# Performance work log

Hardware: AMD Instinct MI355X
Metric: run time of the kernel (lower is better)

The kernel has to match this reference:

```python
import math
import jax, jax.numpy as jnp
import numpy as np

OLEN = 512
RATIO = 0.5
DROP_P = 0.2


def _gat(x, src, dst, W, a_s, a_d, b):
    """PyG GATConv (heads=1, concat=True, add_self_loops=True, neg_slope=0.2)."""
    n = x.shape[0]
    loops = jnp.arange(n, dtype=src.dtype)
    s = jnp.concatenate([src, loops])  # [E+N] source nodes
    d = jnp.concatenate([dst, loops])  # [E+N] destination nodes
    h = x @ W                           # [N, H]
    alpha_s = h @ a_s                   # [N]
    alpha_d = h @ a_d                   # [N]
    e = jax.nn.leaky_relu(alpha_s[s] + alpha_d[d], 0.2)  # [E+N]
    # segment softmax over destination neighborhoods
    m = jax.ops.segment_max(e, d, num_segments=n)
    ee = jnp.exp(e - m[d])
    denom = jax.ops.segment_sum(ee, d, num_segments=n)
    alpha = ee / denom[d]
    out = jax.ops.segment_sum(alpha[:, None] * h[s], d, num_segments=n)
    return out + b


def _forward(x, src, dst, W1, a_src1, a_dst1, b1, W2, a_src2, a_dst2, b2,
             W3, a_src3, a_dst3, b3, W_rel, W_root, b_pool):
    N, E = x.shape[0], src.shape[0]
    key = jax.random.key(42)
    h = x
    for i, (W, a_s, a_d, b) in enumerate([(W1, a_src1, a_dst1, b1),
                                          (W2, a_src2, a_dst2, b2),
                                          (W3, a_src3, a_dst3, b3)]):
        h = jax.nn.relu(_gat(h, src, dst, W, a_s, a_d, b))
        keep = jax.random.bernoulli(jax.random.fold_in(key, i), 1.0 - DROP_P, h.shape)
        h = jnp.where(keep, h / (1.0 - DROP_P), 0.0)  # F.dropout(training=True)

    # SAGPooling(GraphConv score, ratio=0.5, tanh) repeated until n <= 512.
    # Node counts are static per iteration (k = ceil(0.5*n)); edge arrays keep
    # fixed size E with a validity mask (edges dropped when an endpoint is pooled away).
    cur_src, cur_dst = src, dst
    emask = jnp.ones((E,), dtype=h.dtype)
    n = N
    while True:
        agg = jax.ops.segment_sum(h[cur_src] * emask[:, None], cur_dst, num_segments=n)
        score = (agg @ W_rel + h @ W_root + b_pool)[:, 0]  # GraphConv(d->1), aggr='add'
        score = jnp.tanh(score)
        k = math.ceil(RATIO * n)
        top_vals, perm = jax.lax.top_k(score, k)
        h = h[perm] * top_vals[:, None]
        inv = jnp.full((n,), -1, dtype=cur_src.dtype).at[perm].set(
            jnp.arange(k, dtype=cur_src.dtype))
        ns, nd = inv[cur_src], inv[cur_dst]
        valid = (ns >= 0) & (nd >= 0)
        emask = emask * valid.astype(emask.dtype)
        cur_src = jnp.where(valid, ns, 0)
        cur_dst = jnp.where(valid, nd, 0)
        n = k
        if n <= OLEN:
            break

    out = jnp.zeros((OLEN, h.shape[1]), h.dtype).at[:n].set(h)
    return out


def setup_inputs() -> dict:
    key = jax.random.key(0)
    ks = jax.random.split(key, 20)
    N, E, IDIM, HDIM = 50000, 800000, 128, 200
    inp = {
        "x": jax.random.normal(ks[0], (N, IDIM), jnp.float32),
        "src": jax.random.randint(ks[1], (E,), 0, N, jnp.int32),
        "dst": jax.random.randint(ks[2], (E,), 0, N, jnp.int32),
    }
    def w(k, shape, fan_in):
        return jax.random.normal(k, shape, jnp.float32) / np.sqrt(fan_in).astype(np.float32)
    inp["W1"] = w(ks[3], (IDIM, HDIM), IDIM)
    inp["a_src1"] = w(ks[4], (HDIM,), HDIM)
    inp["a_dst1"] = w(ks[5], (HDIM,), HDIM)
    inp["b1"] = jnp.zeros((HDIM,), jnp.float32)
    inp["W2"] = w(ks[6], (HDIM, HDIM), HDIM)
    inp["a_src2"] = w(ks[7], (HDIM,), HDIM)
    inp["a_dst2"] = w(ks[8], (HDIM,), HDIM)
    inp["b2"] = jnp.zeros((HDIM,), jnp.float32)
    inp["W3"] = w(ks[9], (HDIM, HDIM), HDIM)
    inp["a_src3"] = w(ks[10], (HDIM,), HDIM)
    inp["a_dst3"] = w(ks[11], (HDIM,), HDIM)
    inp["b3"] = jnp.zeros((HDIM,), jnp.float32)
    inp["W_rel"] = w(ks[12], (HDIM, 1), HDIM)
    inp["W_root"] = w(ks[13], (HDIM, 1), HDIM)
    inp["b_pool"] = jnp.zeros((1,), jnp.float32)
    return inp


def reference(x, src, dst, W1, a_src1, a_dst1, b1, W2, a_src2, a_dst2, b2,
              W3, a_src3, a_dst3, b3, W_rel, W_root, b_pool):
    return _forward(x, src, dst, W1, a_src1, a_dst1, b1, W2, a_src2, a_dst2, b2,
                    W3, a_src3, a_dst3, b3, W_rel, W_root, b_pool)
```

## Files before the change

kernel.cpp:

```cpp
#include <hip/hip_runtime.h>
#include <cstdint>
#include <cstddef>


__host__ __device__ inline void tf_round(uint32_t &x0, uint32_t &x1, int r) {
  x0 += x1;
  x1 = (x1 << r) | (x1 >> (32 - r));
  x1 ^= x0;
}

__host__ __device__ inline void threefry2x32(uint32_t k0, uint32_t k1,
                                             uint32_t &x0, uint32_t &x1) {
  uint32_t ks2 = k0 ^ k1 ^ 0x1BD11BDAu;
  x0 += k0; x1 += k1;
  tf_round(x0, x1, 13); tf_round(x0, x1, 15); tf_round(x0, x1, 26); tf_round(x0, x1, 6);
  x0 += k1; x1 += ks2 + 1u;
  tf_round(x0, x1, 17); tf_round(x0, x1, 29); tf_round(x0, x1, 16); tf_round(x0, x1, 24);
  x0 += ks2; x1 += k0 + 2u;
  tf_round(x0, x1, 13); tf_round(x0, x1, 15); tf_round(x0, x1, 26); tf_round(x0, x1, 6);
  x0 += k0; x1 += k1 + 3u;
  tf_round(x0, x1, 17); tf_round(x0, x1, 29); tf_round(x0, x1, 16); tf_round(x0, x1, 24);
  x0 += k1; x1 += ks2 + 4u;
  tf_round(x0, x1, 13); tf_round(x0, x1, 15); tf_round(x0, x1, 26); tf_round(x0, x1, 6);
  x0 += ks2; x1 += k0 + 5u;
}

__global__ __launch_bounds__(256) void gemm200_k(
    const float* __restrict__ A, const float* __restrict__ B,
    float* __restrict__ C, int M, int K) {
  __shared__ float As[128 * 9];
  __shared__ __align__(16) float Bs[8][208];
  int tid = threadIdx.x;
  int m0 = blockIdx.x * 128;
  int r = tid >> 2;
  int colBase = (tid & 3) * 52;
  int nq = (colBase == 156) ? 11 : 13;
  float acc0[52], acc1[52];
#pragma unroll
  for (int q = 0; q < 52; q++) { acc0[q] = 0.f; acc1[q] = 0.f; }

  int arow = tid >> 1;
  int ac = (tid & 1) * 4;
  int gmA = m0 + arow;
  const float* Aptr = A + (size_t)gmA * K + ac;
  int bk0 = tid / 50, bc0 = (tid - bk0 * 50) * 4;
  int t2 = tid + 256;
  int bk1 = t2 / 50, bc1 = (t2 - bk1 * 50) * 4;
  bool hasB1 = (t2 < 400);

  float4 va = make_float4(0.f, 0.f, 0.f, 0.f);
  if (gmA < M) va = *(const float4*)(Aptr);
  float4 vb0 = *(const float4*)(B + (size_t)bk0 * 200 + bc0);
  float4 vb1 = make_float4(0.f, 0.f, 0.f, 0.f);
  if (hasB1) vb1 = *(const float4*)(B + (size_t)bk1 * 200 + bc1);

  for (int k0 = 0; k0 < K; k0 += 8) {
    As[arow * 9 + ac + 0] = va.x;
    As[arow * 9 + ac + 1] = va.y;
    As[arow * 9 + ac + 2] = va.z;
    As[arow * 9 + ac + 3] = va.w;
    *(float4*)(&Bs[bk0][bc0]) = vb0;
    if (hasB1) *(float4*)(&Bs[bk1][bc1]) = vb1;
    __syncthreads();
    int kn = k0 + 8;
    if (kn < K) {
      if (gmA < M) va = *(const float4*)(Aptr + kn);
      vb0 = *(const float4*)(B + (size_t)(kn + bk0) * 200 + bc0);
      if (hasB1) vb1 = *(const float4*)(B + (size_t)(kn + bk1) * 200 + bc1);
    }
#pragma unroll
    for (int kk = 0; kk < 8; kk++) {
      float a0 = As[r * 9 + kk];
      float a1 = As[(r + 64) * 9 + kk];
#pragma unroll
      for (int q = 0; q < 13; q++) {
        float4 b = *(const float4*)(&Bs[kk][colBase + 4 * q]);
        acc0[4 * q + 0] += a0 * b.x; acc0[4 * q + 1] += a0 * b.y;
        acc0[4 * q + 2] += a0 * b.z; acc0[4 * q + 3] += a0 * b.w;
        acc1[4 * q + 0] += a1 * b.x; acc1[4 * q + 1] += a1 * b.y;
        acc1[4 * q + 2] += a1 * b.z; acc1[4 * q + 3] += a1 * b.w;
      }
    }
    __syncthreads();
  }
  int gm0 = m0 + r, gm1 = m0 + r + 64;
#pragma unroll
  for (int q = 0; q < 13; q++) {
    if (q < nq) {
      int col = colBase + 4 * q;
      float4 v0 = make_float4(acc0[4 * q + 0], acc0[4 * q + 1],
                              acc0[4 * q + 2], acc0[4 * q + 3]);
      float4 v1 = make_float4(acc1[4 * q + 0], acc1[4 * q + 1],
                              acc1[4 * q + 2], acc1[4 * q + 3]);
      if (gm0 < M) *(float4*)(C + (size_t)gm0 * 200 + col) = v0;
      if (gm1 < M) *(float4*)(C + (size_t)gm1 * 200 + col) = v1;
    }
  }
}

__global__ __launch_bounds__(256) void dual_dot_k(
    const float* __restrict__ H, const float* __restrict__ v1,
    const float* __restrict__ v2, float* __restrict__ o1,
    float* __restrict__ o2, int n) {
  int wave = blockIdx.x * 4 + (threadIdx.x >> 6);
  int lane = threadIdx.x & 63;
  if (wave >= n) return;
  const float* row = H + (size_t)wave * 200;
  float s1 = 0.f, s2 = 0.f;
  for (int d = lane; d < 200; d += 64) {
    float h = row[d];
    s1 += h * v1[d];
    s2 += h * v2[d];
  }
  for (int off = 32; off; off >>= 1) {
    s1 += __shfl_down(s1, off);
    s2 += __shfl_down(s2, off);
  }
  if (lane == 0) { o1[wave] = s1; o2[wave] = s2; }
}

__global__ __launch_bounds__(256) void indeg_k(const int* __restrict__ dst,
                                               int* __restrict__ cnt, int E) {
  int e = blockIdx.x * 256 + threadIdx.x;
  if (e < E) atomicAdd(&cnt[dst[e]], 1);
}

__global__ __launch_bounds__(256) void scan_k(const int* __restrict__ cnt,
                                              int* __restrict__ rowptr, int N) {
  __shared__ int psum[256];
  int t = threadIdx.x;
  int CH = (N + 255) / 256;
  int beg = t * CH, end = min(beg + CH, N);
  if (beg > N) { beg = N; }
  int s = 0;
  for (int i = beg; i < end; i++) s += cnt[i];
  psum[t] = s;
  __syncthreads();
  if (t == 0) {
    int run = 0;
    for (int i = 0; i < 256; i++) { int v = psum[i]; psum[i] = run; run += v; }
  }
  __syncthreads();
  int run = psum[t];
  for (int i = beg; i < end; i++) { rowptr[i] = run; run += cnt[i]; }
  if (end == N && beg <= N) rowptr[N] = run;
}

__global__ __launch_bounds__(256) void cpyint_k(const int* __restrict__ a,
                                                int* __restrict__ b, int n) {
  int i = blockIdx.x * 256 + threadIdx.x;
  if (i < n) b[i] = a[i];
}

__global__ __launch_bounds__(256) void place_k(const int* __restrict__ dst,
                                               int* __restrict__ curs,
                                               int* __restrict__ csr, int E) {
  int e = blockIdx.x * 256 + threadIdx.x;
  if (e >= E) return;
  int pos = atomicAdd(&curs[dst[e]], 1);
  csr[pos] = e;
}

__global__ __launch_bounds__(256) void sortrow_k(const int* __restrict__ rowptr,
                                                 int* __restrict__ csr, int N) {
  int d = blockIdx.x * 256 + threadIdx.x;
  if (d >= N) return;
  int b = rowptr[d], e2 = rowptr[d + 1];
  for (int i = b + 1; i < e2; i++) {
    int v = csr[i];
    int j = i - 1;
    while (j >= b && csr[j] > v) { csr[j + 1] = csr[j]; j--; }
    csr[j + 1] = v;
  }
}

__device__ inline float dec_ord(unsigned enc) {
  unsigned b = (enc & 0x80000000u) ? (enc ^ 0x80000000u) : ~enc;
  return __uint_as_float(b);
}

__global__ __launch_bounds__(256) void edge_max_k(
    const int* __restrict__ src, const int* __restrict__ dst,
    const float* __restrict__ as_, const float* __restrict__ ad_,
    unsigned* __restrict__ menc, int E, int N) {
  int j = blockIdx.x * 256 + threadIdx.x;
  if (j >= E + N) return;
  int s, d;
  if (j < E) { s = src[j]; d = dst[j]; } else { s = j - E; d = s; }
  float v = as_[s] + ad_[d];
  float ev = (v >= 0.f) ? v : 0.2f * v;
  unsigned b = __float_as_uint(ev);
  unsigned enc = (b & 0x80000000u) ? ~b : (b | 0x80000000u);
  atomicMax(&menc[d], enc);
}

__global__ __launch_bounds__(256) void ee_k(
    const int* __restrict__ src, const int* __restrict__ dst,
    const float* __restrict__ as_, const float* __restrict__ ad_,
    const unsigned* __restrict__ menc, float* __restrict__ ee, int E, int N) {
  int j = blockIdx.x * 256 + threadIdx.x;
  if (j >= E + N) return;
  int s, d;
  if (j < E) { s = src[j]; d = dst[j]; } else { s = j - E; d = s; }
  float v = as_[s] + ad_[d];
  float ev = (v >= 0.f) ? v : 0.2f * v;
  ee[j] = expf(ev - dec_ord(menc[d]));
}

__global__ __launch_bounds__(256) void den_k(const int* __restrict__ rowptr,
                                             const int* __restrict__ csr,
                                             const float* __restrict__ ee,
                                             float* __restrict__ den, int E, int N) {
  int d = blockIdx.x * 256 + threadIdx.x;
  if (d >= N) return;
  float s = 0.f;
  int b = rowptr[d], e2 = rowptr[d + 1];
  for (int i = b; i < e2; i++) s = __fadd_rn(s, ee[csr[i]]);
  s = __fadd_rn(s, ee[E + d]);
  den[d] = s;
}

__global__ __launch_bounds__(256) void alpha_k(const int* __restrict__ dst,
                                               const float* __restrict__ den,
                                               float* __restrict__ ee, int E, int N) {
  int j = blockIdx.x * 256 + threadIdx.x;
  if (j >= E + N) return;
  int d = (j < E) ? dst[j] : (j - E);
  ee[j] = ee[j] / den[d];
}

__global__ __launch_bounds__(256) void gat_out_k(
    const int* __restrict__ rowptr, const int* __restrict__ csr,
    const int* __restrict__ src, const float* __restrict__ alpha,
    const float* __restrict__ HW, float* __restrict__ OUT, int E, int N) {
  int node = blockIdx.x * 4 + (threadIdx.x >> 6);
  int lane = threadIdx.x & 63;
  if (node >= N || lane >= 50) return;
  int b = rowptr[node];
  int deg = rowptr[node + 1] - b;
  int cnt = deg + 1;

  auto fetchS = [&](int t, int &s, float &w) {
    if (t < deg) {
      int e = csr[b + t];
      s = src[e];
      w = alpha[e];
    } else if (t == deg) {
      s = node;
      w = alpha[E + node];
    } else {
      s = node;
      w = 0.f;
    }
  };

  int s0, s1, s2;
  float w0, w1, w2;
  fetchS(0, s0, w0);
  fetchS(1, s1, w1);
  fetchS(2, s2, w2);
  float4 h0 = *(const float4*)(HW + (size_t)s0 * 200 + 4 * lane);
  float4 h1 = *(const float4*)(HW + (size_t)s1 * 200 + 4 * lane);
  float4 acc = make_float4(0.f, 0.f, 0.f, 0.f);
  for (int t = 0; t < cnt; t++) {
    int s3;
    float w3;
    fetchS(t + 3, s3, w3);
    float4 h2 = *(const float4*)(HW + (size_t)s2 * 200 + 4 * lane);
    acc.x = __fadd_rn(acc.x, __fmul_rn(w0, h0.x));
    acc.y = __fadd_rn(acc.y, __fmul_rn(w0, h0.y));
    acc.z = __fadd_rn(acc.z, __fmul_rn(w0, h0.z));
    acc.w = __fadd_rn(acc.w, __fmul_rn(w0, h0.w));
    h0 = h1; h1 = h2;
    w0 = w1; w1 = w2; w2 = w3;
    s2 = s3;
  }
  *(float4*)(OUT + (size_t)node * 200 + 4 * lane) = acc;
}

__global__ __launch_bounds__(256) void epi_k(float* __restrict__ H,
                                             const float* __restrict__ bias,
                                             uint32_t k0, uint32_t k1, int total) {
  int t = blockIdx.x * 256 + threadIdx.x;
  if (t >= total) return;
  uint32_t x0 = 0u, x1 = (uint32_t)t;
  threefry2x32(k0, k1, x0, x1);
  uint32_t bits = x0 ^ x1;
  float u = __uint_as_float((bits >> 9) | 0x3f800000u) - 1.0f;
  int col = t % 200;
  float v = H[t] + bias[col];
  v = fmaxf(v, 0.f);
  H[t] = (u < 0.8f) ? (v / 0.8f) : 0.f;
}

__global__ __launch_bounds__(256) void einit_k(
    const int* __restrict__ src, const int* __restrict__ dst,
    int* __restrict__ cs, int* __restrict__ cd, int* __restrict__ orig,
    int E, int N) {
  int e = blockIdx.x * 256 + threadIdx.x;
  if (e < E) { cs[e] = src[e]; cd[e] = dst[e]; }
  if (e < N) orig[e] = e;
}

__global__ __launch_bounds__(256) void pool_agg_k(
    const int* __restrict__ rowptr, const int* __restrict__ csr,
    const int* __restrict__ csrc, const int* __restrict__ orig,
    const float* __restrict__ H, float* __restrict__ AGG, int n) {
  int node = blockIdx.x * 4 + (threadIdx.x >> 6);
  int lane = threadIdx.x & 63;
  if (node >= n || lane >= 50) return;
  int o = orig[node];
  int b = rowptr[o];
  int deg = rowptr[o + 1] - b;

  auto fetchS = [&](int t, int &s, float &w) {
    if (t < deg) {
      int e = csr[b + t];
      int sv = csrc[e];
      s = (sv >= 0) ? sv : 0;
      w = (sv >= 0) ? 1.f : 0.f;
    } else {
      s = 0;
      w = 0.f;
    }
  };

  int s0, s1, s2;
  float w0, w1, w2;
  fetchS(0, s0, w0);
  fetchS(1, s1, w1);
  fetchS(2, s2, w2);
  float4 h0 = *(const float4*)(H + (size_t)s0 * 200 + 4 * lane);
  float4 h1 = *(const float4*)(H + (size_t)s1 * 200 + 4 * lane);
  float4 acc = make_float4(0.f, 0.f, 0.f, 0.f);
  for (int t = 0; t < deg; t++) {
    int s3;
    float w3;
    fetchS(t + 3, s3, w3);
    float4 h2 = *(const float4*)(H + (size_t)s2 * 200 + 4 * lane);
    acc.x = __fadd_rn(acc.x, __fmul_rn(w0, h0.x));
    acc.y = __fadd_rn(acc.y, __fmul_rn(w0, h0.y));
    acc.z = __fadd_rn(acc.z, __fmul_rn(w0, h0.z));
    acc.w = __fadd_rn(acc.w, __fmul_rn(w0, h0.w));
    h0 = h1; h1 = h2;
    w0 = w1; w1 = w2; w2 = w3;
    s2 = s3;
  }
  *(float4*)(AGG + (size_t)node * 200 + 4 * lane) = acc;
}

__global__ __launch_bounds__(256) void score2_k(
    const float* __restrict__ AGG, const float* __restrict__ H,
    const float* __restrict__ wrel, const float* __restrict__ wroot,
    const float* __restrict__ bp, float* __restrict__ score, int n) {
  int node = blockIdx.x * 4 + (threadIdx.x >> 6);
  int lane = threadIdx.x & 63;
  if (node >= n) return;
  const float* arow = AGG + (size_t)node * 200;
  const float* hrow = H + (size_t)node * 200;
  float s1 = 0.f, s2 = 0.f;
  for (int d = lane; d < 200; d += 64) {
    s1 += arow[d] * wrel[d];
    s2 += hrow[d] * wroot[d];
  }
  for (int off = 32; off; off >>= 1) {
    s1 += __shfl_down(s1, off);
    s2 += __shfl_down(s2, off);
  }
  if (lane == 0) score[node] = tanhf((s1 + s2) + bp[0]);
}


__global__ __launch_bounds__(256) void rhenc_k(const float* __restrict__ score,
                                               unsigned* __restrict__ keyA,
                                               int* __restrict__ payA,
                                               int* __restrict__ counts,
                                               int n, int NB) {
  __shared__ int hist[256];
  hist[threadIdx.x] = 0;
  __syncthreads();
  int i = blockIdx.x * 256 + threadIdx.x;
  if (i < n) {
    unsigned b = __float_as_uint(score[i]);
    if (b == 0x80000000u) b = 0u;
    unsigned enc = (b & 0x80000000u) ? ~b : (b | 0x80000000u);
    unsigned key = ~enc;
    keyA[i] = key;
    payA[i] = i;
    atomicAdd(&hist[key & 255u], 1);
  }
  __syncthreads();
  counts[threadIdx.x * NB + blockIdx.x] = hist[threadIdx.x];
}

__global__ __launch_bounds__(256) void rhist_k(const unsigned* __restrict__ key,
                                               int* __restrict__ counts,
                                               int n, int NB, int shift) {
  __shared__ int hist[256];
  hist[threadIdx.x] = 0;
  __syncthreads();
  int i = blockIdx.x * 256 + threadIdx.x;
  if (i < n) atomicAdd(&hist[(key[i] >> shift) & 255u], 1);
  __syncthreads();
  counts[threadIdx.x * NB + blockIdx.x] = hist[threadIdx.x];
}

__global__ __launch_bounds__(256) void rscan_k(const int* __restrict__ counts,
                                               int* __restrict__ base, int NB) {
  __shared__ int tot[256];
  int t = threadIdx.x;
  int s = 0;
  for (int b = 0; b < NB; b++) s += counts[t * NB + b];
  tot[t] = s;
  __syncthreads();
  if (t == 0) {
    int run = 0;
    for (int i = 0; i < 256; i++) { int v = tot[i]; tot[i] = run; run += v; }
  }
  __syncthreads();
  int run = tot[t];
  for (int b = 0; b < NB; b++) { base[t * NB + b] = run; run += counts[t * NB + b]; }
}

__global__ __launch_bounds__(256) void rscatter_k(
    const unsigned* __restrict__ keyIn, const int* __restrict__ payIn,
    const int* __restrict__ base, unsigned* __restrict__ keyOut,
    int* __restrict__ payOut, int n, int NB, int shift) {
  __shared__ int dig[256];
  int t = threadIdx.x;
  int i = blockIdx.x * 256 + t;
  unsigned k = 0u;
  int p = 0, d = -1;
  if (i < n) {
    k = keyIn[i];
    p = payIn[i];
    d = (int)((k >> shift) & 255u);
  }
  dig[t] = d;
  __syncthreads();
  if (i < n) {
    int local = 0;
    for (int j = 0; j < t; j++) local += (dig[j] == d) ? 1 : 0;
    int pos = base[d * NB + blockIdx.x] + local;
    keyOut[pos] = k;
    payOut[pos] = p;
  }
}

__global__ __launch_bounds__(256) void rscatterF_k(
    const unsigned* __restrict__ keyIn, const int* __restrict__ payIn,
    const int* __restrict__ base, const int* __restrict__ oin,
    int* __restrict__ oout, int* __restrict__ perm, int* __restrict__ inv,
    int n, int NB, int k) {
  __shared__ int dig[256];
  int t = threadIdx.x;
  int i = blockIdx.x * 256 + t;
  int p = 0, d = -1;
  if (i < n) {
    p = payIn[i];
    d = (int)((keyIn[i] >> 24) & 255u);
  }
  dig[t] = d;
  __syncthreads();
  if (i < n) {
    int local = 0;
    for (int j = 0; j < t; j++) local += (dig[j] == d) ? 1 : 0;
    int pos = base[d * NB + blockIdx.x] + local;
    if (pos < k) { perm[pos] = p; inv[p] = pos; oout[pos] = oin[p]; }
    else inv[p] = -1;
  }
}

__global__ __launch_bounds__(256) void gather_k(
    const float* __restrict__ H, const int* __restrict__ perm,
    const float* __restrict__ score, float* __restrict__ Ho, int k) {
  int r = blockIdx.x;
  int d = threadIdx.x;
  int p = perm[r];
  float s = score[p];
  if (d < 200) Ho[(size_t)r * 200 + d] = __fmul_rn(H[(size_t)p * 200 + d], s);
}

__global__ __launch_bounds__(256) void remap_k(int* __restrict__ cs,
                                               int* __restrict__ cd,
                                               const int* __restrict__ inv, int E) {
  int e = blockIdx.x * 256 + threadIdx.x;
  if (e >= E) return;
  int a = cs[e];
  if (a < 0) return;
  int na = inv[a], nb = inv[cd[e]];
  bool valid = (na >= 0) && (nb >= 0);
  cs[e] = valid ? na : -1;
  cd[e] = valid ? nb : -1;
}

__global__ __launch_bounds__(256) void out_copy_k(const float* __restrict__ h,
                                                  float* __restrict__ out, int cnt) {
  int t = blockIdx.x * 256 + threadIdx.x;
  if (t < cnt) out[t] = h[t];
}

extern "C" void kernel_launch(void* const* d_in, const int* in_sizes, int n_in,
                              void* d_out, int out_size, void* d_ws, size_t ws_size,
                              hipStream_t stream) {
  const int ID = 128, HD = 200;
  const int N = in_sizes[0] / ID;
  const int E = in_sizes[1];
  const int ET = E + N;
  const int total = N * HD;

  const float* x = (const float*)d_in[0];
  const int* src = (const int*)d_in[1];
  const int* dst = (const int*)d_in[2];
  const float* W[3]   = {(const float*)d_in[3], (const float*)d_in[7], (const float*)d_in[11]};
  const float* asv[3] = {(const float*)d_in[4], (const float*)d_in[8], (const float*)d_in[12]};
  const float* adv[3] = {(const float*)d_in[5], (const float*)d_in[9], (const float*)d_in[13]};
  const float* bv[3]  = {(const float*)d_in[6], (const float*)d_in[10], (const float*)d_in[14]};
  const float* Wrel  = (const float*)d_in[15];
  const float* Wroot = (const float*)d_in[16];
  const float* bpool = (const float*)d_in[17];

  char* ws = (char*)d_ws;
  float*    bufA  = (float*)(ws + 0);
  float*    bufB  = (float*)(ws + 40000000);
  float*    as_   = (float*)(ws + 80000000);
  float*    ad_   = (float*)(ws + 80200000);
  float*    ee_   = (float*)(ws + 80400000);
  unsigned* menc  = (unsigned*)(ws + 83800000);
  float*    den   = (float*)(ws + 84000000);
  float*    score = (float*)(ws + 84200000);
  int*      rank_ = (int*)(ws + 84400000);
  int*      perm_ = (int*)(ws + 84600000);
  int*      inv_  = (int*)(ws + 84800000);
  int*      origA = (int*)(ws + 85000000);
  int*      origB = (int*)(ws + 85200000);
  int*      rowptr= (int*)(ws + 85400000);
  int*      curs  = (int*)(ws + 85650000);
  int*      csr   = (int*)(ws + 85850000);
  int*      csrc  = (int*)(ws + 89050000);
  int*      cdst  = (int*)(ws + 92250000);

  char* rx = ws + 80400000;
  unsigned* keyA   = (unsigned*)(rx + 0 * 262144);
  unsigned* keyB   = (unsigned*)(rx + 1 * 262144);
  int*      payA   = (int*)(rx + 2 * 262144);
  int*      payB   = (int*)(rx + 3 * 262144);
  int*      rcounts= (int*)(rx + 4 * 262144);
  int*      rbase  = (int*)(rx + 5 * 262144);

  uint32_t fk0[3], fk1[3];
  for (int i = 0; i < 3; i++) {
    uint32_t a = 0u, b = (uint32_t)i;
    threefry2x32(0u, 42u, a, b);
    fk0[i] = a; fk1[i] = b;
  }

  const int B256 = 256;
  hipMemsetAsync(rank_, 0, (size_t)N * 4, stream);
  indeg_k<<<(E + 255) / 256, B256, 0, stream>>>(dst, rank_, E);
  scan_k<<<1, B256, 0, stream>>>(rank_, rowptr, N);
  cpyint_k<<<(N + 255) / 256, B256, 0, stream>>>(rowptr, curs, N);
  place_k<<<(E + 255) / 256, B256, 0, stream>>>(dst, curs, csr, E);
  sortrow_k<<<(N + 255) / 256, B256, 0, stream>>>(rowptr, csr, N);

  for (int i = 0; i < 3; i++) {
    const float* in = (i == 0) ? x : bufB;
    int K = (i == 0) ? ID : HD;
    gemm200_k<<<(N + 127) / 128, B256, 0, stream>>>(in, W[i], bufA, N, K);
    dual_dot_k<<<(N + 3) / 4, B256, 0, stream>>>(bufA, asv[i], adv[i], as_, ad_, N);
    hipMemsetAsync(menc, 0, (size_t)N * 4, stream);
    edge_max_k<<<(ET + 255) / 256, B256, 0, stream>>>(src, dst, as_, ad_, menc, E, N);
    ee_k<<<(ET + 255) / 256, B256, 0, stream>>>(src, dst, as_, ad_, menc, ee_, E, N);
    den_k<<<(N + 255) / 256, B256, 0, stream>>>(rowptr, csr, ee_, den, E, N);
    alpha_k<<<(ET + 255) / 256, B256, 0, stream>>>(dst, den, ee_, E, N);
    gat_out_k<<<(N + 3) / 4, B256, 0, stream>>>(rowptr, csr, src, ee_, bufA, bufB, E, N);
    epi_k<<<(total + 255) / 256, B256, 0, stream>>>(bufB, bv[i], fk0[i], fk1[i], total);
  }

  einit_k<<<(E + 255) / 256, B256, 0, stream>>>(src, dst, csrc, cdst, origA, E, N);
  float* hcur = bufB;
  float* hnext = bufA;
  int* ocur = origA;
  int* onext = origB;
  int n = N;
  while (true) {
    int k = (n + 1) / 2;
    int NB = (n + 255) / 256;
    pool_agg_k<<<(n + 3) / 4, B256, 0, stream>>>(rowptr, csr, csrc, ocur, hcur, hnext, n);
    score2_k<<<(n + 3) / 4, B256, 0, stream>>>(hnext, hcur, Wrel, Wroot, bpool, score, n);
    rhenc_k<<<NB, B256, 0, stream>>>(score, keyA, payA, rcounts, n, NB);
    rscan_k<<<1, B256, 0, stream>>>(rcounts, rbase, NB);
    rscatter_k<<<NB, B256, 0, stream>>>(keyA, payA, rbase, keyB, payB, n, NB, 0);
    rhist_k<<<NB, B256, 0, stream>>>(keyB, rcounts, n, NB, 8);
    rscan_k<<<1, B256, 0, stream>>>(rcounts, rbase, NB);
    rscatter_k<<<NB, B256, 0, stream>>>(keyB, payB, rbase, keyA, payA, n, NB, 8);
    rhist_k<<<NB, B256, 0, stream>>>(keyA, rcounts, n, NB, 16);
    rscan_k<<<1, B256, 0, stream>>>(rcounts, rbase, NB);
    rscatter_k<<<NB, B256, 0, stream>>>(keyA, payA, rbase, keyB, payB, n, NB, 16);
    rhist_k<<<NB, B256, 0, stream>>>(keyB, rcounts, n, NB, 24);
    rscan_k<<<1, B256, 0, stream>>>(rcounts, rbase, NB);
    rscatterF_k<<<NB, B256, 0, stream>>>(keyB, payB, rbase, ocur, onext, perm_, inv_,
                                         n, NB, k);
    gather_k<<<k, B256, 0, stream>>>(hcur, perm_, score, hnext, k);
    remap_k<<<(E + 255) / 256, B256, 0, stream>>>(csrc, cdst, inv_, E);
    { float* t = hcur; hcur = hnext; hnext = t; }
    { int* t = ocur; ocur = onext; onext = t; }
    n = k;
    if (n <= 512) break;
  }

  hipMemsetAsync(d_out, 0, (size_t)out_size * 4, stream);
  out_copy_k<<<(n * HD + 255) / 256, B256, 0, stream>>>(hcur, (float*)d_out, n * HD);
}
```

Measured before the change: 2.625 ms.

## Fuse alpha normalization into aggregation, deepen gather prefetch, fuse radix histograms into scatter

The separate alpha_k division pass is removed; gat_out_k now divides each edge's exp value by the per-node denominator inline. Both gather-aggregation kernels switch from a 3-deep software pipeline to an 8-wide, double-buffered prefetch so more row loads are in flight per wave. The radix sort's separate histogram kernels are removed: each scatter pass atomically builds the next digit's counts, and the scan zeroes counts for reuse. This saves launches and memory passes, at the cost of more registers (lower occupancy) and global atomics in the scatter.

```diff
diff --git a/kernel.cpp b/kernel.cpp
--- a/kernel.cpp
+++ b/kernel.cpp
@@ -220,60 +220,66 @@
   den[d] = s;
 }
 
-__global__ __launch_bounds__(256) void alpha_k(const int* __restrict__ dst,
-                                               const float* __restrict__ den,
-                                               float* __restrict__ ee, int E, int N) {
-  int j = blockIdx.x * 256 + threadIdx.x;
-  if (j >= E + N) return;
-  int d = (j < E) ? dst[j] : (j - E);
-  ee[j] = ee[j] / den[d];
-}
+#define GLD(s) (*(const float4*)(Hl + (size_t)(s) * 200))
+#define ACC(W_, H_)                                    \
+  acc.x = __fadd_rn(acc.x, __fmul_rn((W_), (H_).x));   \
+  acc.y = __fadd_rn(acc.y, __fmul_rn((W_), (H_).y));   \
+  acc.z = __fadd_rn(acc.z, __fmul_rn((W_), (H_).z));   \
+  acc.w = __fadd_rn(acc.w, __fmul_rn((W_), (H_).w));
 
 __global__ __launch_bounds__(256) void gat_out_k(
     const int* __restrict__ rowptr, const int* __restrict__ csr,
-    const int* __restrict__ src, const float* __restrict__ alpha,
-    const float* __restrict__ HW, float* __restrict__ OUT, int E, int N) {
+    const int* __restrict__ src, const float* __restrict__ ee,
+    const float* __restrict__ den, const float* __restrict__ HW,
+    float* __restrict__ OUT, int E, int N) {
   int node = blockIdx.x * 4 + (threadIdx.x >> 6);
   int lane = threadIdx.x & 63;
   if (node >= N || lane >= 50) return;
   int b = rowptr[node];
   int deg = rowptr[node + 1] - b;
   int cnt = deg + 1;
-
-  auto fetchS = [&](int t, int &s, float &w) {
+  float dn = den[node];
+  const float* __restrict__ Hl = HW + 4 * lane;
+
+  auto fS = [&](int t, int &s, float &w) {
     if (t < deg) {
       int e = csr[b + t];
       s = src[e];
-      w = alpha[e];
+      w = __fdiv_rn(ee[e], dn);
     } else if (t == deg) {
       s = node;
-      w = alpha[E + node];
+      w = __fdiv_rn(ee[E + node], dn);
     } else {
       s = node;
       w = 0.f;
     }
   };
 
-  int s0, s1, s2;
-  float w0, w1, w2;
-  fetchS(0, s0, w0);
-  fetchS(1, s1, w1);
-  fetchS(2, s2, w2);
-  float4 h0 = *(const float4*)(HW + (size_t)s0 * 200 + 4 * lane);
-  float4 h1 = *(const float4*)(HW + (size_t)s1 * 200 + 4 * lane);
+  int sx0, sx1, sx2, sx3, sy0, sy1, sy2, sy3;
+  float wcx0, wcx1, wcx2, wcx3, wcy0, wcy1, wcy2, wcy3;
+  float wx0, wx1, wx2, wx3, wy0, wy1, wy2, wy3;
+
+  fS(0, sx0, wcx0); fS(1, sx1, wcx1); fS(2, sx2, wcx2); fS(3, sx3, wcx3);
+  fS(4, sy0, wcy0); fS(5, sy1, wcy1); fS(6, sy2, wcy2); fS(7, sy3, wcy3);
+  float4 hx0 = GLD(sx0), hx1 = GLD(sx1), hx2 = GLD(sx2), hx3 = GLD(sx3);
+  float4 hy0 = GLD(sy0), hy1 = GLD(sy1), hy2 = GLD(sy2), hy3 = GLD(sy3);
+  fS(8, sx0, wx0); fS(9, sx1, wx1); fS(10, sx2, wx2); fS(11, sx3, wx3);
+  fS(12, sy0, wy0); fS(13, sy1, wy1); fS(14, sy2, wy2); fS(15, sy3, wy3);
+
   float4 acc = make_float4(0.f, 0.f, 0.f, 0.f);
-  for (int t = 0; t < cnt; t++) {
-    int s3;
-    float w3;
-    fetchS(t + 3, s3, w3);
-    float4 h2 = *(const float4*)(HW + (size_t)s2 * 200 + 4 * lane);
-    acc.x = __fadd_rn(acc.x, __fmul_rn(w0, h0.x));
-    acc.y = __fadd_rn(acc.y, __fmul_rn(w0, h0.y));
-    acc.z = __fadd_rn(acc.z, __fmul_rn(w0, h0.z));
-    acc.w = __fadd_rn(acc.w, __fmul_rn(w0, h0.w));
-    h0 = h1; h1 = h2;
-    w0 = w1; w1 = w2; w2 = w3;
-    s2 = s3;
+  int nit = (cnt + 7) / 8;
+  for (int j = 0; j < nit; j++) {
+    int s8 = j * 8;
+    ACC(wcx0, hx0); ACC(wcx1, hx1); ACC(wcx2, hx2); ACC(wcx3, hx3);
+    hx0 = GLD(sx0); hx1 = GLD(sx1); hx2 = GLD(sx2); hx3 = GLD(sx3);
+    wcx0 = wx0; wcx1 = wx1; wcx2 = wx2; wcx3 = wx3;
+    fS(s8 + 16, sx0, wx0); fS(s8 + 17, sx1, wx1);
+    fS(s8 + 18, sx2, wx2); fS(s8 + 19, sx3, wx3);
+    ACC(wcy0, hy0); ACC(wcy1, hy1); ACC(wcy2, hy2); ACC(wcy3, hy3);
+    hy0 = GLD(sy0); hy1 = GLD(sy1); hy2 = GLD(sy2); hy3 = GLD(sy3);
+    wcy0 = wy0; wcy1 = wy1; wcy2 = wy2; wcy3 = wy3;
+    fS(s8 + 20, sy0, wy0); fS(s8 + 21, sy1, wy1);
+    fS(s8 + 22, sy2, wy2); fS(s8 + 23, sy3, wy3);
   }
   *(float4*)(OUT + (size_t)node * 200 + 4 * lane) = acc;
 }
@@ -312,8 +318,9 @@
   int o = orig[node];
   int b = rowptr[o];
   int deg = rowptr[o + 1] - b;
-
-  auto fetchS = [&](int t, int &s, float &w) {
+  const float* __restrict__ Hl = H + 4 * lane;
+
+  auto fS = [&](int t, int &s, float &w) {
     if (t < deg) {
       int e = csr[b + t];
       int sv = csrc[e];
@@ -325,29 +332,36 @@
     }
   };
 
-  int s0, s1, s2;
-  float w0, w1, w2;
-  fetchS(0, s0, w0);
-  fetchS(1, s1, w1);
-  fetchS(2, s2, w2);
-  float4 h0 = *(const float4*)(H + (size_t)s0 * 200 + 4 * lane);
-  float4 h1 = *(const float4*)(H + (size_t)s1 * 200 + 4 * lane);
+  int sx0, sx1, sx2, sx3, sy0, sy1, sy2, sy3;
+  float wcx0, wcx1, wcx2, wcx3, wcy0, wcy1, wcy2, wcy3;
+  float wx0, wx1, wx2, wx3, wy0, wy1, wy2, wy3;
+
+  fS(0, sx0, wcx0); fS(1, sx1, wcx1); fS(2, sx2, wcx2); fS(3, sx3, wcx3);
+  fS(4, sy0, wcy0); fS(5, sy1, wcy1); fS(6, sy2, wcy2); fS(7, sy3, wcy3);
+  float4 hx0 = GLD(sx0), hx1 = GLD(sx1), hx2 = GLD(sx2), hx3 = GLD(sx3);
+  float4 hy0 = GLD(sy0), hy1 = GLD(sy1), hy2 = GLD(sy2), hy3 = GLD(sy3);
+  fS(8, sx0, wx0); fS(9, sx1, wx1); fS(10, sx2, wx2); fS(11, sx3, wx3);
+  fS(12, sy0, wy0); fS(13, sy1, wy1); fS(14, sy2, wy2); fS(15, sy3, wy3);
+
   float4 acc = make_float4(0.f, 0.f, 0.f, 0.f);
-  for (int t = 0; t < deg; t++) {
-    int s3;
-    float w3;
-    fetchS(t + 3, s3, w3);
-    float4 h2 = *(const float4*)(H + (size_t)s2 * 200 + 4 * lane);
-    acc.x = __fadd_rn(acc.x, __fmul_rn(w0, h0.x));
-    acc.y = __fadd_rn(acc.y, __fmul_rn(w0, h0.y));
-    acc.z = __fadd_rn(acc.z, __fmul_rn(w0, h0.z));
-    acc.w = __fadd_rn(acc.w, __fmul_rn(w0, h0.w));
-    h0 = h1; h1 = h2;
-    w0 = w1; w1 = w2; w2 = w3;
-    s2 = s3;
+  int nit = (deg + 7) / 8;
+  for (int j = 0; j < nit; j++) {
+    int s8 = j * 8;
+    ACC(wcx0, hx0); ACC(wcx1, hx1); ACC(wcx2, hx2); ACC(wcx3, hx3);
+    hx0 = GLD(sx0); hx1 = GLD(sx1); hx2 = GLD(sx2); hx3 = GLD(sx3);
+    wcx0 = wx0; wcx1 = wx1; wcx2 = wx2; wcx3 = wx3;
+    fS(s8 + 16, sx0, wx0); fS(s8 + 17, sx1, wx1);
+    fS(s8 + 18, sx2, wx2); fS(s8 + 19, sx3, wx3);
+    ACC(wcy0, hy0); ACC(wcy1, hy1); ACC(wcy2, hy2); ACC(wcy3, hy3);
+    hy0 = GLD(sy0); hy1 = GLD(sy1); hy2 = GLD(sy2); hy3 = GLD(sy3);
+    wcy0 = wy0; wcy1 = wy1; wcy2 = wy2; wcy3 = wy3;
+    fS(s8 + 20, sy0, wy0); fS(s8 + 21, sy1, wy1);
+    fS(s8 + 22, sy2, wy2); fS(s8 + 23, sy3, wy3);
   }
   *(float4*)(AGG + (size_t)node * 200 + 4 * lane) = acc;
 }
+#undef GLD
+#undef ACC
 
 __global__ __launch_bounds__(256) void score2_k(
     const float* __restrict__ AGG, const float* __restrict__ H,
@@ -393,19 +407,7 @@
   counts[threadIdx.x * NB + blockIdx.x] = hist[threadIdx.x];
 }
 
-__global__ __launch_bounds__(256) void rhist_k(const unsigned* __restrict__ key,
-                                               int* __restrict__ counts,
-                                               int n, int NB, int shift) {
-  __shared__ int hist[256];
-  hist[threadIdx.x] = 0;
-  __syncthreads();
-  int i = blockIdx.x * 256 + threadIdx.x;
-  if (i < n) atomicAdd(&hist[(key[i] >> shift) & 255u], 1);
-  __syncthreads();
-  counts[threadIdx.x * NB + blockIdx.x] = hist[threadIdx.x];
-}
-
-__global__ __launch_bounds__(256) void rscan_k(const int* __restrict__ counts,
+__global__ __launch_bounds__(256) void rscan_k(int* __restrict__ counts,
                                                int* __restrict__ base, int NB) {
   __shared__ int tot[256];
   int t = threadIdx.x;
@@ -419,13 +421,19 @@
   }
   __syncthreads();
   int run = tot[t];
-  for (int b = 0; b < NB; b++) { base[t * NB + b] = run; run += counts[t * NB + b]; }
+  for (int b = 0; b < NB; b++) {
+    int c = counts[t * NB + b];
+    base[t * NB + b] = run;
+    run += c;
+    counts[t * NB + b] = 0;
+  }
 }
 
 __global__ __launch_bounds__(256) void rscatter_k(
     const unsigned* __restrict__ keyIn, const int* __restrict__ payIn,
     const int* __restrict__ base, unsigned* __restrict__ keyOut,
-    int* __restrict__ payOut, int n, int NB, int shift) {
+    int* __restrict__ payOut, int* __restrict__ countsNext,
+    int n, int NB, int shift) {
   __shared__ int dig[256];
   int t = threadIdx.x;
   int i = blockIdx.x * 256 + t;
@@ -444,6 +452,8 @@
     int pos = base[d * NB + blockIdx.x] + local;
     keyOut[pos] = k;
     payOut[pos] = p;
+    int nd = (int)((k >> (shift + 8)) & 255u);
+    atomicAdd(&countsNext[nd * NB + (pos >> 8)], 1);
   }
 }
 
@@ -572,8 +582,7 @@
     edge_max_k<<<(ET + 255) / 256, B256, 0, stream>>>(src, dst, as_, ad_, menc, E, N);
     ee_k<<<(ET + 255) / 256, B256, 0, stream>>>(src, dst, as_, ad_, menc, ee_, E, N);
     den_k<<<(N + 255) / 256, B256, 0, stream>>>(rowptr, csr, ee_, den, E, N);
-    alpha_k<<<(ET + 255) / 256, B256, 0, stream>>>(dst, den, ee_, E, N);
-    gat_out_k<<<(N + 3) / 4, B256, 0, stream>>>(rowptr, csr, src, ee_, bufA, bufB, E, N);
+    gat_out_k<<<(N + 3) / 4, B256, 0, stream>>>(rowptr, csr, src, ee_, den, bufA, bufB, E, N);
     epi_k<<<(total + 255) / 256, B256, 0, stream>>>(bufB, bv[i], fk0[i], fk1[i], total);
   }
 
@@ -590,14 +599,11 @@
     score2_k<<<(n + 3) / 4, B256, 0, stream>>>(hnext, hcur, Wrel, Wroot, bpool, score, n);
     rhenc_k<<<NB, B256, 0, stream>>>(score, keyA, payA, rcounts, n, NB);
     rscan_k<<<1, B256, 0, stream>>>(rcounts, rbase, NB);
-    rscatter_k<<<NB, B256, 0, stream>>>(keyA, payA, rbase, keyB, payB, n, NB, 0);
-    rhist_k<<<NB, B256, 0, stream>>>(keyB, rcounts, n, NB, 8);
+    rscatter_k<<<NB, B256, 0, stream>>>(keyA, payA, rbase, keyB, payB, rcounts, n, NB, 0);
     rscan_k<<<1, B256, 0, stream>>>(rcounts, rbase, NB);
-    rscatter_k<<<NB, B256, 0, stream>>>(keyB, payB, rbase, keyA, payA, n, NB, 8);
-    rhist_k<<<NB, B256, 0, stream>>>(keyA, rcounts, n, NB, 16);
+    rscatter_k<<<NB, B256, 0, stream>>>(keyB, payB, rbase, keyA, payA, rcounts, n, NB, 8);
     rscan_k<<<1, B256, 0, stream>>>(rcounts, rbase, NB);
-    rscatter_k<<<NB, B256, 0, stream>>>(keyA, payA, rbase, keyB, payB, n, NB, 16);
-    rhist_k<<<NB, B256, 0, stream>>>(keyB, rcounts, n, NB, 24);
+    rscatter_k<<<NB, B256, 0, stream>>>(keyA, payA, rbase, keyB, payB, rcounts, n, NB, 16);
     rscan_k<<<1, B256, 0, stream>>>(rcounts, rbase, NB);
     rscatterF_k<<<NB, B256, 0, stream>>>(keyB, payB, rbase, ocur, onext, perm_, inv_,
                                          n, NB, k);
```

Result: slower. 3.445 ms (+31.2%).
